# Optimization experiments

Measured on AMD Instinct MI355X. Metric: run time of the kernel, lower is better.

Reference implementation:

```python
import jax, jax.numpy as jnp
import numpy as np

WIN = 7       # window_size (square)
SHIFT = 3     # shift_size
HEADS = 4
WS = WIN * WIN  # 49 tokens per window


def _rel_index():
    # Swin relative position index, shape (WS*WS,), static ints
    coords = np.stack(np.meshgrid(np.arange(WIN), np.arange(WIN), indexing='ij'))
    cf = coords.reshape(2, -1)
    rel = (cf[:, :, None] - cf[:, None, :]).transpose(1, 2, 0)  # (WS, WS, 2)
    rel[:, :, 0] += WIN - 1
    rel[:, :, 1] += WIN - 1
    rel[:, :, 0] *= 2 * WIN - 1
    return rel.sum(-1).reshape(-1)

_REL_IDX = jnp.asarray(_rel_index())


def _attn_mask(H, W):
    # shift mask per window, shape (num_windows, WS, WS), static
    m = np.zeros((H, W), np.float32)
    cnt = 0
    for h in ((0, -WIN), (-WIN, -SHIFT), (-SHIFT, None)):
        for w in ((0, -WIN), (-WIN, -SHIFT), (-SHIFT, None)):
            m[h[0]:h[1], w[0]:w[1]] = cnt
            cnt += 1
    m = m.reshape(H // WIN, WIN, W // WIN, WIN).transpose(0, 2, 1, 3).reshape(-1, WS)
    diff = m[:, None, :] - m[:, :, None]
    return np.where(diff == 0, 0.0, -100.0).astype(np.float32)


def setup_inputs() -> dict:
    key = jax.random.key(0)
    ks = jax.random.split(key, 6)
    C = 128
    return {
        'x': jax.random.normal(ks[0], (64, 56, 56, C), jnp.float32),
        'qkv_kernel': jax.random.normal(ks[1], (C, 3 * C), jnp.float32) * (C ** -0.5),
        'qkv_bias': jax.random.normal(ks[2], (3 * C,), jnp.float32) * 0.02,
        'proj_kernel': jax.random.normal(ks[3], (C, C), jnp.float32) * (C ** -0.5),
        'proj_bias': jax.random.normal(ks[4], (C,), jnp.float32) * 0.02,
        'rel_pos_table': jax.random.normal(ks[5], ((2 * WIN - 1) ** 2, HEADS), jnp.float32) * 0.02,
    }


def reference(x, qkv_kernel, qkv_bias, proj_kernel, proj_bias, rel_pos_table):
    B, H, W, C = x.shape
    nH, nW = H // WIN, W // WIN
    head_dim = C // HEADS

    # cyclic shift + window partition -> (B*nH*nW, WS, C)
    xs = jnp.roll(x, (-SHIFT, -SHIFT), axis=(1, 2))
    xw = xs.reshape(B, nH, WIN, nW, WIN, C).transpose(0, 1, 3, 2, 4, 5).reshape(B * nH * nW, WS, C)

    qkv = xw @ qkv_kernel + qkv_bias
    qkv = qkv.reshape(-1, WS, 3, HEADS, head_dim).transpose(2, 0, 3, 1, 4)  # (3, n, h, WS, d)
    q, k, v = qkv[0], qkv[1], qkv[2]

    attn = jnp.einsum('nhsd,nhtd->nhst', q * head_dim ** -0.5, k)

    # relative position bias: (1, heads, WS, WS)
    bias = rel_pos_table[_REL_IDX].reshape(WS, WS, HEADS).transpose(2, 0, 1)[None]
    attn = attn + bias

    # shift mask (static)
    mask = jnp.asarray(_attn_mask(H, W))  # (nH*nW, WS, WS)
    attn = attn.reshape(B, nH * nW, HEADS, WS, WS) + mask[None, :, None]
    attn = jax.nn.softmax(attn.reshape(-1, HEADS, WS, WS), axis=-1)

    out = jnp.einsum('nhst,nhtd->nhsd', attn, v).transpose(0, 2, 1, 3).reshape(-1, WS, C)
    out = out @ proj_kernel + proj_bias

    # window merge + reverse shift
    out = out.reshape(B, nH, nW, WIN, WIN, C).transpose(0, 1, 3, 2, 4, 5).reshape(B, H, W, C)
    return jnp.roll(out, (SHIFT, SHIFT), axis=(1, 2))
```

## Files before the change

### kernel.cpp

```cpp
#include <hip/hip_runtime.h>
#include <hip/hip_bf16.h>

#define WIN 7
#define SHIFT_SZ 3
#define HEADS 4
#define WSQ 49
#define CH 128
#define HW 56

typedef short s16x8 __attribute__((ext_vector_type(8)));
typedef float f32x4 __attribute__((ext_vector_type(4)));


__global__ void prep_weights(const float* __restrict__ qkv_kernel,
                             const float* __restrict__ proj_kernel,
                             __hip_bfloat16* __restrict__ ws) {
  int idx = blockIdx.x * 256 + threadIdx.x;
  if (idx < 49152) {
    int n = idx >> 7, c = idx & 127;
    ws[idx] = __float2bfloat16(qkv_kernel[c * 384 + n]);
  }
  if (idx < 16384) {
    int n = idx >> 7, c = idx & 127;
    ws[49152 + idx] = __float2bfloat16(proj_kernel[c * 128 + n]);
  }
}

__global__ void prep_tbl(const float* __restrict__ rel_pos_table,
                         __hip_bfloat16* __restrict__ tbl) {
  int idx = blockIdx.x * 256 + threadIdx.x;
  int t = idx & 63;
  int s = (idx >> 6) & 63;
  int h = (idx >> 12) & 3;
  int win = idx >> 14;
  float v;
  if (t >= WSQ) v = -30000.f;
  else if (s >= WSQ) v = 0.f;
  else {
    int i1 = s / 7, j1 = s % 7, i2 = t / 7, j2 = t % 7;
    int ridx = (i1 - i2 + 6) * 13 + (j1 - j2 + 6);
    float bias = rel_pos_table[ridx * HEADS + h];
    int wy = win >> 3, wx = win & 7;
    int rh1 = (wy < 7) ? 0 : (i1 < 4 ? 1 : 2);
    int rh2 = (wy < 7) ? 0 : (i2 < 4 ? 1 : 2);
    int rw1 = (wx < 7) ? 0 : (j1 < 4 ? 1 : 2);
    int rw2 = (wx < 7) ? 0 : (j2 < 4 ? 1 : 2);
    float mask = (rh1 == rh2 && rw1 == rw2) ? 0.f : -100.f;
    v = bias + mask;
  }
  tbl[idx] = __float2bfloat16(v);
}


__launch_bounds__(512, 4)
__global__ void swin_attn(const float* __restrict__ x,
                          const float* __restrict__ qkv_bias,
                          const float* __restrict__ proj_bias,
                          const __hip_bfloat16* __restrict__ wqkvT,
                          const __hip_bfloat16* __restrict__ wprojT,
                          const __hip_bfloat16* __restrict__ tbl,
                          float* __restrict__ out) {
  __shared__ __align__(16) char smem[76800];
  __hip_bfloat16* a_lds  = (__hip_bfloat16*)smem;
  __hip_bfloat16* qk_lds = (__hip_bfloat16*)(smem + 17408);
  __hip_bfloat16* p_lds  = qk_lds;
  __hip_bfloat16* vt_lds = (__hip_bfloat16*)(smem + 58368);

  const int tid = threadIdx.x;
  const int lane = tid & 63;
  const int wv = tid >> 6;
  const int g = lane >> 4;
  const int c = lane & 15;

  const int widx = blockIdx.x;
  const int b  = widx >> 6;
  const int wy = (widx >> 3) & 7;
  const int wx = widx & 7;
  const int win64 = widx & 63;

  for (int it = tid; it < 1024; it += 512) {
    int s = it >> 4;
    int l16 = it & 15;
    union { s16x8 v; __hip_bfloat16 h[8]; } u;
    if (s < WSQ) {
      int i = s / 7, j = s - i * 7;
      int hh = wy * 7 + i + SHIFT_SZ; if (hh >= HW) hh -= HW;
      int ww = wx * 7 + j + SHIFT_SZ; if (ww >= HW) ww -= HW;
      const float4* src = (const float4*)(x + (((b * HW + hh) * HW + ww) * CH + l16 * 8));
      float4 f0 = src[0], f1 = src[1];
      u.h[0] = __float2bfloat16(f0.x); u.h[1] = __float2bfloat16(f0.y);
      u.h[2] = __float2bfloat16(f0.z); u.h[3] = __float2bfloat16(f0.w);
      u.h[4] = __float2bfloat16(f1.x); u.h[5] = __float2bfloat16(f1.y);
      u.h[6] = __float2bfloat16(f1.z); u.h[7] = __float2bfloat16(f1.w);
    } else {
      #pragma unroll
      for (int q = 0; q < 8; ++q) u.h[q] = __float2bfloat16(0.f);
    }
    *(s16x8*)(a_lds + s * 136 + l16 * 8) = u.v;
  }
  __syncthreads();

  {
    f32x4 acc[4][3];
    #pragma unroll
    for (int mt = 0; mt < 4; ++mt)
      #pragma unroll
      for (int ntl = 0; ntl < 3; ++ntl) acc[mt][ntl] = (f32x4){0.f, 0.f, 0.f, 0.f};

    #pragma unroll
    for (int kt = 0; kt < 4; ++kt) {
      s16x8 af[4];
      #pragma unroll
      for (int mt = 0; mt < 4; ++mt)
        af[mt] = *(const s16x8*)(a_lds + (16 * mt + c) * 136 + kt * 32 + g * 8);
      #pragma unroll
      for (int ntl = 0; ntl < 3; ++ntl) {
        int nt = 3 * wv + ntl;
        s16x8 bf = *(const s16x8*)(wqkvT + (16 * nt + c) * 128 + kt * 32 + g * 8);
        #pragma unroll
        for (int mt = 0; mt < 4; ++mt)
          acc[mt][ntl] = __builtin_amdgcn_mfma_f32_16x16x32_bf16(af[mt], bf, acc[mt][ntl], 0, 0, 0);
      }
    }
    #pragma unroll
    for (int ntl = 0; ntl < 3; ++ntl) {
      int nt = 3 * wv + ntl;
      int n = 16 * nt + c;
      float bias = qkv_bias[n];
      int sel = n >> 7;
      int rem = n & 127;
      int head = rem >> 5;
      int d = rem & 31;
      #pragma unroll
      for (int mt = 0; mt < 4; ++mt)
        #pragma unroll
        for (int r = 0; r < 4; ++r) {
          int s = 16 * mt + 4 * g + r;
          float v = acc[mt][ntl][r] + bias;
          if (sel == 0)
            qk_lds[(head * 64 + s) * 40 + d] = __float2bfloat16(v * 0.17677669529663687f);
          else if (sel == 1)
            qk_lds[10240 + (head * 64 + s) * 40 + d] = __float2bfloat16(v);
          else
            vt_lds[(head * 32 + d) * 72 + s] = __float2bfloat16(v);
        }
    }
  }
  __syncthreads();

  const int h = wv >> 1;
  const int mh = wv & 1;
  float den[2][4];
  f32x4 oacc[2][2];
  {
    s16x8 qf[2], kf[4];
    #pragma unroll
    for (int m = 0; m < 2; ++m)
      qf[m] = *(const s16x8*)(qk_lds + (h * 64 + 16 * (2 * mh + m) + c) * 40 + g * 8);
    #pragma unroll
    for (int nt = 0; nt < 4; ++nt)
      kf[nt] = *(const s16x8*)(qk_lds + 10240 + (h * 64 + 16 * nt + c) * 40 + g * 8);
    __syncthreads();

    f32x4 sacc[2][4];
    #pragma unroll
    for (int m = 0; m < 2; ++m)
      #pragma unroll
      for (int nt = 0; nt < 4; ++nt) {
        sacc[m][nt] = (f32x4){0.f, 0.f, 0.f, 0.f};
        sacc[m][nt] = __builtin_amdgcn_mfma_f32_16x16x32_bf16(qf[m], kf[nt], sacc[m][nt], 0, 0, 0);
      }

    const __hip_bfloat16* tb = tbl + (((win64 << 2) + h) << 12);
    #pragma unroll
    for (int m = 0; m < 2; ++m)
      #pragma unroll
      for (int nt = 0; nt < 4; ++nt)
        #pragma unroll
        for (int r = 0; r < 4; ++r) {
          int s = 16 * (2 * mh + m) + 4 * g + r;
          int t = 16 * nt + c;
          sacc[m][nt][r] += __bfloat162float(tb[(s << 6) + t]);
        }
    #pragma unroll
    for (int m = 0; m < 2; ++m)
      #pragma unroll
      for (int r = 0; r < 4; ++r) {
        float mx = fmaxf(fmaxf(sacc[m][0][r], sacc[m][1][r]), fmaxf(sacc[m][2][r], sacc[m][3][r]));
        #pragma unroll
        for (int off = 1; off < 16; off <<= 1) mx = fmaxf(mx, __shfl_xor(mx, off));
        float sum = 0.f;
        #pragma unroll
        for (int nt = 0; nt < 4; ++nt) {
          float e = __expf(sacc[m][nt][r] - mx);
          sacc[m][nt][r] = e;
          sum += e;
        }
        #pragma unroll
        for (int off = 1; off < 16; off <<= 1) sum += __shfl_xor(sum, off);
        den[m][r] = sum;
      }
    #pragma unroll
    for (int m = 0; m < 2; ++m)
      #pragma unroll
      for (int nt = 0; nt < 4; ++nt)
        #pragma unroll
        for (int r = 0; r < 4; ++r) {
          int s = 16 * (2 * mh + m) + 4 * g + r;
          int t = 16 * nt + c;
          p_lds[(h * 64 + s) * 72 + t] = __float2bfloat16(sacc[m][nt][r]);
        }
  }
  __syncthreads();

  #pragma unroll
  for (int m = 0; m < 2; ++m)
    #pragma unroll
    for (int ntd = 0; ntd < 2; ++ntd) oacc[m][ntd] = (f32x4){0.f, 0.f, 0.f, 0.f};
  #pragma unroll
  for (int kt = 0; kt < 2; ++kt) {
    s16x8 pf[2];
    #pragma unroll
    for (int m = 0; m < 2; ++m)
      pf[m] = *(const s16x8*)(p_lds + (h * 64 + 16 * (2 * mh + m) + c) * 72 + kt * 32 + g * 8);
    #pragma unroll
    for (int ntd = 0; ntd < 2; ++ntd) {
      s16x8 vf = *(const s16x8*)(vt_lds + (h * 32 + 16 * ntd + c) * 72 + kt * 32 + g * 8);
      #pragma unroll
      for (int m = 0; m < 2; ++m)
        oacc[m][ntd] = __builtin_amdgcn_mfma_f32_16x16x32_bf16(pf[m], vf, oacc[m][ntd], 0, 0, 0);
    }
  }
  #pragma unroll
  for (int m = 0; m < 2; ++m)
    #pragma unroll
    for (int ntd = 0; ntd < 2; ++ntd)
      #pragma unroll
      for (int r = 0; r < 4; ++r) {
        int s = 16 * (2 * mh + m) + 4 * g + r;
        int col = h * 32 + 16 * ntd + c;
        a_lds[s * 136 + col] = __float2bfloat16(oacc[m][ntd][r] / den[m][r]);
      }
  __syncthreads();

  {
    f32x4 pacc[4];
    #pragma unroll
    for (int mt = 0; mt < 4; ++mt) pacc[mt] = (f32x4){0.f, 0.f, 0.f, 0.f};
    #pragma unroll
    for (int kt = 0; kt < 4; ++kt) {
      s16x8 bfp = *(const s16x8*)(wprojT + (16 * wv + c) * 128 + kt * 32 + g * 8);
      #pragma unroll
      for (int mt = 0; mt < 4; ++mt) {
        s16x8 afo = *(const s16x8*)(a_lds + (16 * mt + c) * 136 + kt * 32 + g * 8);
        pacc[mt] = __builtin_amdgcn_mfma_f32_16x16x32_bf16(afo, bfp, pacc[mt], 0, 0, 0);
      }
    }
    float pb = proj_bias[16 * wv + c];
    #pragma unroll
    for (int mt = 0; mt < 4; ++mt)
      #pragma unroll
      for (int r = 0; r < 4; ++r) {
        int s = 16 * mt + 4 * g + r;
        if (s < WSQ) {
          int i = s / 7, j = s - i * 7;
          int hh = wy * 7 + i + SHIFT_SZ; if (hh >= HW) hh -= HW;
          int ww = wx * 7 + j + SHIFT_SZ; if (ww >= HW) ww -= HW;
          out[((b * HW + hh) * HW + ww) * CH + 16 * wv + c] = pacc[mt][r] + pb;
        }
      }
  }
}

extern "C" void kernel_launch(void* const* d_in, const int* in_sizes, int n_in,
                              void* d_out, int out_size, void* d_ws, size_t ws_size,
                              hipStream_t stream) {
  const float* x            = (const float*)d_in[0];
  const float* qkv_kernel   = (const float*)d_in[1];
  const float* qkv_bias     = (const float*)d_in[2];
  const float* proj_kernel  = (const float*)d_in[3];
  const float* proj_bias    = (const float*)d_in[4];
  const float* rel_pos_tbl  = (const float*)d_in[5];
  float* out = (float*)d_out;

  __hip_bfloat16* wsb    = (__hip_bfloat16*)d_ws;
  __hip_bfloat16* wqkvT  = wsb;
  __hip_bfloat16* wprojT = wsb + 49152;
  __hip_bfloat16* tbl    = wsb + 65536;

  prep_weights<<<dim3(192), dim3(256), 0, stream>>>(qkv_kernel, proj_kernel, wsb);
  prep_tbl<<<dim3(4096), dim3(256), 0, stream>>>(rel_pos_tbl, tbl);
  swin_attn<<<dim3(4096), dim3(512), 0, stream>>>(x, qkv_bias, proj_bias,
                                                  wqkvT, wprojT, tbl, out);
}
```

Before: 155.7 us.

## Transpose MFMA operand roles, shrink LDS, use exp2 softmax with folded scales

The QKV projection now computes Q/K transposed (weights as the A operand), so results are written to LDS as packed 4-element vectors. V^T uses an XOR-swizzled layout to avoid bank conflicts, and the projection output is stored as float4. Softmax runs per row inside a lane with only two cross-lane shuffles, uses exp2 with log2e folded into the q scale and the bias table, and normalises P before PV instead of dividing the output. The bias table is stored transposed. The LDS footprint is reduced from 76800 to 54272 bytes so the launch bound can rise to 6 blocks per CU. In exchange, bf16 rounding of the normalised probabilities shifts slightly.

```diff
diff --git a/kernel.cpp b/kernel.cpp
--- a/kernel.cpp
+++ b/kernel.cpp
@@ -3,12 +3,14 @@
 
 #define WIN 7
 #define SHIFT_SZ 3
-#define HEADS 4
 #define WSQ 49
 #define CH 128
 #define HW 56
+#define LOG2E 1.4426950408889634f
+#define QSCALE (0.17677669529663687f * LOG2E)
 
 typedef short s16x8 __attribute__((ext_vector_type(8)));
+typedef short s16x4 __attribute__((ext_vector_type(4)));
 typedef float f32x4 __attribute__((ext_vector_type(4)));
 
 
@@ -29,30 +31,37 @@
 __global__ void prep_tbl(const float* __restrict__ rel_pos_table,
                          __hip_bfloat16* __restrict__ tbl) {
   int idx = blockIdx.x * 256 + threadIdx.x;
-  int t = idx & 63;
-  int s = (idx >> 6) & 63;
+  int s = idx & 63;
+  int t = (idx >> 6) & 63;
   int h = (idx >> 12) & 3;
   int win = idx >> 14;
   float v;
-  if (t >= WSQ) v = -30000.f;
+  if (t >= WSQ) v = -43280.f;
   else if (s >= WSQ) v = 0.f;
   else {
     int i1 = s / 7, j1 = s % 7, i2 = t / 7, j2 = t % 7;
     int ridx = (i1 - i2 + 6) * 13 + (j1 - j2 + 6);
-    float bias = rel_pos_table[ridx * HEADS + h];
+    float bias = rel_pos_table[ridx * 4 + h];
     int wy = win >> 3, wx = win & 7;
     int rh1 = (wy < 7) ? 0 : (i1 < 4 ? 1 : 2);
     int rh2 = (wy < 7) ? 0 : (i2 < 4 ? 1 : 2);
     int rw1 = (wx < 7) ? 0 : (j1 < 4 ? 1 : 2);
     int rw2 = (wx < 7) ? 0 : (j2 < 4 ? 1 : 2);
     float mask = (rh1 == rh2 && rw1 == rw2) ? 0.f : -100.f;
-    v = bias + mask;
+    v = (bias + mask) * LOG2E;
   }
   tbl[idx] = __float2bfloat16(v);
 }
 
 
-__launch_bounds__(512, 4)
+static __device__ __forceinline__ s16x8 ld2x64(const __hip_bfloat16* p) {
+  s16x8 r;
+  *(s16x4*)&r = *(const s16x4*)p;
+  *(((s16x4*)&r) + 1) = *(const s16x4*)(p + 4);
+  return r;
+}
+
+__launch_bounds__(512, 6)
 __global__ void swin_attn(const float* __restrict__ x,
                           const float* __restrict__ qkv_bias,
                           const float* __restrict__ proj_bias,
@@ -60,11 +69,13 @@
                           const __hip_bfloat16* __restrict__ wprojT,
                           const __hip_bfloat16* __restrict__ tbl,
                           float* __restrict__ out) {
-  __shared__ __align__(16) char smem[76800];
+  __shared__ __align__(16) char smem[54272];
   __hip_bfloat16* a_lds  = (__hip_bfloat16*)smem;
-  __hip_bfloat16* qk_lds = (__hip_bfloat16*)(smem + 17408);
-  __hip_bfloat16* p_lds  = qk_lds;
-  __hip_bfloat16* vt_lds = (__hip_bfloat16*)(smem + 58368);
+  __hip_bfloat16* q_lds  = (__hip_bfloat16*)smem;
+  __hip_bfloat16* k_lds  = (__hip_bfloat16*)(smem + 18432);
+  __hip_bfloat16* vt_lds = (__hip_bfloat16*)(smem + 36864);
+  __hip_bfloat16* p_lds  = (__hip_bfloat16*)smem;
+  __hip_bfloat16* o_lds  = (__hip_bfloat16*)(smem + 36864);
 
   const int tid = threadIdx.x;
   const int lane = tid & 63;
@@ -100,135 +111,144 @@
   }
   __syncthreads();
 
+  f32x4 acc_qk[2][4];
+  f32x4 acc_v[4];
+  #pragma unroll
+  for (int ntl = 0; ntl < 2; ++ntl)
+    #pragma unroll
+    for (int mt = 0; mt < 4; ++mt) acc_qk[ntl][mt] = (f32x4){0.f, 0.f, 0.f, 0.f};
+  #pragma unroll
+  for (int mt = 0; mt < 4; ++mt) acc_v[mt] = (f32x4){0.f, 0.f, 0.f, 0.f};
+
+  #pragma unroll
+  for (int kt = 0; kt < 4; ++kt) {
+    s16x8 af[4];
+    #pragma unroll
+    for (int mt = 0; mt < 4; ++mt)
+      af[mt] = *(const s16x8*)(a_lds + (16 * mt + c) * 136 + kt * 32 + g * 8);
+    #pragma unroll
+    for (int ntl = 0; ntl < 2; ++ntl) {
+      s16x8 bf = *(const s16x8*)(wqkvT + (16 * (2 * wv + ntl) + c) * 128 + kt * 32 + g * 8);
+      #pragma unroll
+      for (int mt = 0; mt < 4; ++mt)
+        acc_qk[ntl][mt] = __builtin_amdgcn_mfma_f32_16x16x32_bf16(bf, af[mt], acc_qk[ntl][mt], 0, 0, 0);
+    }
+    s16x8 bv = *(const s16x8*)(wqkvT + (16 * (16 + wv) + c) * 128 + kt * 32 + g * 8);
+    #pragma unroll
+    for (int mt = 0; mt < 4; ++mt)
+      acc_v[mt] = __builtin_amdgcn_mfma_f32_16x16x32_bf16(af[mt], bv, acc_v[mt], 0, 0, 0);
+  }
+  __syncthreads();
+
   {
-    f32x4 acc[4][3];
-    #pragma unroll
-    for (int mt = 0; mt < 4; ++mt)
-      #pragma unroll
-      for (int ntl = 0; ntl < 3; ++ntl) acc[mt][ntl] = (f32x4){0.f, 0.f, 0.f, 0.f};
-
-    #pragma unroll
-    for (int kt = 0; kt < 4; ++kt) {
-      s16x8 af[4];
-      #pragma unroll
-      for (int mt = 0; mt < 4; ++mt)
-        af[mt] = *(const s16x8*)(a_lds + (16 * mt + c) * 136 + kt * 32 + g * 8);
-      #pragma unroll
-      for (int ntl = 0; ntl < 3; ++ntl) {
-        int nt = 3 * wv + ntl;
-        s16x8 bf = *(const s16x8*)(wqkvT + (16 * nt + c) * 128 + kt * 32 + g * 8);
-        #pragma unroll
-        for (int mt = 0; mt < 4; ++mt)
-          acc[mt][ntl] = __builtin_amdgcn_mfma_f32_16x16x32_bf16(af[mt], bf, acc[mt][ntl], 0, 0, 0);
+    const float scale = (wv < 4) ? QSCALE : 1.0f;
+    #pragma unroll
+    for (int ntl = 0; ntl < 2; ++ntl) {
+      int qt = 2 * wv + ntl;
+      int h = (qt >> 1) & 3;
+      int d0 = (qt & 1) * 16 + 4 * g;
+      float4 b4 = *(const float4*)(qkv_bias + qt * 16 + 4 * g);
+      __hip_bfloat16* dst = (qt < 8 ? q_lds : k_lds) + h * 64 * 36 + d0;
+      #pragma unroll
+      for (int mt = 0; mt < 4; ++mt) {
+        union { s16x4 v; __hip_bfloat16 h[4]; } u;
+        u.h[0] = __float2bfloat16((acc_qk[ntl][mt][0] + b4.x) * scale);
+        u.h[1] = __float2bfloat16((acc_qk[ntl][mt][1] + b4.y) * scale);
+        u.h[2] = __float2bfloat16((acc_qk[ntl][mt][2] + b4.z) * scale);
+        u.h[3] = __float2bfloat16((acc_qk[ntl][mt][3] + b4.w) * scale);
+        *(s16x4*)(dst + (16 * mt + c) * 36) = u.v;
       }
     }
-    #pragma unroll
-    for (int ntl = 0; ntl < 3; ++ntl) {
-      int nt = 3 * wv + ntl;
-      int n = 16 * nt + c;
-      float bias = qkv_bias[n];
-      int sel = n >> 7;
-      int rem = n & 127;
-      int head = rem >> 5;
-      int d = rem & 31;
-      #pragma unroll
-      for (int mt = 0; mt < 4; ++mt)
-        #pragma unroll
-        for (int r = 0; r < 4; ++r) {
-          int s = 16 * mt + 4 * g + r;
-          float v = acc[mt][ntl][r] + bias;
-          if (sel == 0)
-            qk_lds[(head * 64 + s) * 40 + d] = __float2bfloat16(v * 0.17677669529663687f);
-          else if (sel == 1)
-            qk_lds[10240 + (head * 64 + s) * 40 + d] = __float2bfloat16(v);
-          else
-            vt_lds[(head * 32 + d) * 72 + s] = __float2bfloat16(v);
-        }
-    }
-  }
-  __syncthreads();
-
-  const int h = wv >> 1;
+    int hv = wv >> 1;
+    int d = (wv & 1) * 16 + c;
+    float bv = qkv_bias[256 + wv * 16 + c];
+    __hip_bfloat16* vdst = vt_lds + (hv * 32 + d) * 64;
+    #pragma unroll
+    for (int mt = 0; mt < 4; ++mt) {
+      int s0 = 16 * mt + 4 * g;
+      union { s16x4 v; __hip_bfloat16 h[4]; } u;
+      #pragma unroll
+      for (int r = 0; r < 4; ++r) u.h[r] = __float2bfloat16(acc_v[mt][r] + bv);
+      *(s16x4*)(vdst + (((s0 >> 3) ^ (c & 7)) << 3) + (s0 & 7)) = u.v;
+    }
+  }
+  __syncthreads();
+
+  const int h3 = wv >> 1;
   const int mh = wv & 1;
-  float den[2][4];
+  s16x8 qf[2], kf[4], vf[2][2];
+  #pragma unroll
+  for (int m = 0; m < 2; ++m)
+    qf[m] = ld2x64(q_lds + (h3 * 64 + 16 * (2 * mh + m) + c) * 36 + g * 8);
+  #pragma unroll
+  for (int nt = 0; nt < 4; ++nt)
+    kf[nt] = ld2x64(k_lds + (h3 * 64 + 16 * nt + c) * 36 + g * 8);
+  #pragma unroll
+  for (int kt = 0; kt < 2; ++kt)
+    #pragma unroll
+    for (int ntd = 0; ntd < 2; ++ntd) {
+      int row = h3 * 32 + 16 * ntd + c;
+      int blk = (4 * kt + g) ^ (c & 7);
+      vf[kt][ntd] = *(const s16x8*)(vt_lds + row * 64 + blk * 8);
+    }
+  __syncthreads();
+
+  #pragma unroll
+  for (int m = 0; m < 2; ++m) {
+    f32x4 sc[4];
+    #pragma unroll
+    for (int nt = 0; nt < 4; ++nt) {
+      sc[nt] = (f32x4){0.f, 0.f, 0.f, 0.f};
+      sc[nt] = __builtin_amdgcn_mfma_f32_16x16x32_bf16(kf[nt], qf[m], sc[nt], 0, 0, 0);
+    }
+    const __hip_bfloat16* tb = tbl + (((win64 << 2) + h3) << 12) + 16 * (2 * mh + m) + c;
+    #pragma unroll
+    for (int nt = 0; nt < 4; ++nt)
+      #pragma unroll
+      for (int r = 0; r < 4; ++r)
+        sc[nt][r] += __bfloat162float(tb[(16 * nt + 4 * g + r) << 6]);
+    float mx = -1e30f;
+    #pragma unroll
+    for (int nt = 0; nt < 4; ++nt)
+      #pragma unroll
+      for (int r = 0; r < 4; ++r) mx = fmaxf(mx, sc[nt][r]);
+    mx = fmaxf(mx, __shfl_xor(mx, 16));
+    mx = fmaxf(mx, __shfl_xor(mx, 32));
+    float sum = 0.f;
+    #pragma unroll
+    for (int nt = 0; nt < 4; ++nt)
+      #pragma unroll
+      for (int r = 0; r < 4; ++r) {
+        float e = __builtin_amdgcn_exp2f(sc[nt][r] - mx);
+        sc[nt][r] = e;
+        sum += e;
+      }
+    sum += __shfl_xor(sum, 16);
+    sum += __shfl_xor(sum, 32);
+    float inv = __builtin_amdgcn_rcpf(sum);
+    __hip_bfloat16* prow = p_lds + (h3 * 64 + 16 * (2 * mh + m) + c) * 72;
+    #pragma unroll
+    for (int nt = 0; nt < 4; ++nt) {
+      union { s16x4 v; __hip_bfloat16 h[4]; } u;
+      #pragma unroll
+      for (int r = 0; r < 4; ++r) u.h[r] = __float2bfloat16(sc[nt][r] * inv);
+      *(s16x4*)(prow + 16 * nt + 4 * g) = u.v;
+    }
+  }
+
   f32x4 oacc[2][2];
-  {
-    s16x8 qf[2], kf[4];
-    #pragma unroll
-    for (int m = 0; m < 2; ++m)
-      qf[m] = *(const s16x8*)(qk_lds + (h * 64 + 16 * (2 * mh + m) + c) * 40 + g * 8);
-    #pragma unroll
-    for (int nt = 0; nt < 4; ++nt)
-      kf[nt] = *(const s16x8*)(qk_lds + 10240 + (h * 64 + 16 * nt + c) * 40 + g * 8);
-    __syncthreads();
-
-    f32x4 sacc[2][4];
-    #pragma unroll
-    for (int m = 0; m < 2; ++m)
-      #pragma unroll
-      for (int nt = 0; nt < 4; ++nt) {
-        sacc[m][nt] = (f32x4){0.f, 0.f, 0.f, 0.f};
-        sacc[m][nt] = __builtin_amdgcn_mfma_f32_16x16x32_bf16(qf[m], kf[nt], sacc[m][nt], 0, 0, 0);
-      }
-
-    const __hip_bfloat16* tb = tbl + (((win64 << 2) + h) << 12);
-    #pragma unroll
-    for (int m = 0; m < 2; ++m)
-      #pragma unroll
-      for (int nt = 0; nt < 4; ++nt)
-        #pragma unroll
-        for (int r = 0; r < 4; ++r) {
-          int s = 16 * (2 * mh + m) + 4 * g + r;
-          int t = 16 * nt + c;
-          sacc[m][nt][r] += __bfloat162float(tb[(s << 6) + t]);
-        }
-    #pragma unroll
-    for (int m = 0; m < 2; ++m)
-      #pragma unroll
-      for (int r = 0; r < 4; ++r) {
-        float mx = fmaxf(fmaxf(sacc[m][0][r], sacc[m][1][r]), fmaxf(sacc[m][2][r], sacc[m][3][r]));
-        #pragma unroll
-        for (int off = 1; off < 16; off <<= 1) mx = fmaxf(mx, __shfl_xor(mx, off));
-        float sum = 0.f;
-        #pragma unroll
-        for (int nt = 0; nt < 4; ++nt) {
-          float e = __expf(sacc[m][nt][r] - mx);
-          sacc[m][nt][r] = e;
-          sum += e;
-        }
-        #pragma unroll
-        for (int off = 1; off < 16; off <<= 1) sum += __shfl_xor(sum, off);
-        den[m][r] = sum;
-      }
-    #pragma unroll
-    for (int m = 0; m < 2; ++m)
-      #pragma unroll
-      for (int nt = 0; nt < 4; ++nt)
-        #pragma unroll
-        for (int r = 0; r < 4; ++r) {
-          int s = 16 * (2 * mh + m) + 4 * g + r;
-          int t = 16 * nt + c;
-          p_lds[(h * 64 + s) * 72 + t] = __float2bfloat16(sacc[m][nt][r]);
-        }
-  }
-  __syncthreads();
-
   #pragma unroll
   for (int m = 0; m < 2; ++m)
     #pragma unroll
     for (int ntd = 0; ntd < 2; ++ntd) oacc[m][ntd] = (f32x4){0.f, 0.f, 0.f, 0.f};
   #pragma unroll
   for (int kt = 0; kt < 2; ++kt) {
-    s16x8 pf[2];
-    #pragma unroll
-    for (int m = 0; m < 2; ++m)
-      pf[m] = *(const s16x8*)(p_lds + (h * 64 + 16 * (2 * mh + m) + c) * 72 + kt * 32 + g * 8);
-    #pragma unroll
-    for (int ntd = 0; ntd < 2; ++ntd) {
-      s16x8 vf = *(const s16x8*)(vt_lds + (h * 32 + 16 * ntd + c) * 72 + kt * 32 + g * 8);
-      #pragma unroll
-      for (int m = 0; m < 2; ++m)
-        oacc[m][ntd] = __builtin_amdgcn_mfma_f32_16x16x32_bf16(pf[m], vf, oacc[m][ntd], 0, 0, 0);
+    #pragma unroll
+    for (int m = 0; m < 2; ++m) {
+      s16x8 pf = *(const s16x8*)(p_lds + (h3 * 64 + 16 * (2 * mh + m) + c) * 72 + kt * 32 + g * 8);
+      #pragma unroll
+      for (int ntd = 0; ntd < 2; ++ntd)
+        oacc[m][ntd] = __builtin_amdgcn_mfma_f32_16x16x32_bf16(pf, vf[kt][ntd], oacc[m][ntd], 0, 0, 0);
     }
   }
   #pragma unroll
@@ -236,11 +256,9 @@
     #pragma unroll
     for (int ntd = 0; ntd < 2; ++ntd)
       #pragma unroll
-      for (int r = 0; r < 4; ++r) {
-        int s = 16 * (2 * mh + m) + 4 * g + r;
-        int col = h * 32 + 16 * ntd + c;
-        a_lds[s * 136 + col] = __float2bfloat16(oacc[m][ntd][r] / den[m][r]);
-      }
+      for (int r = 0; r < 4; ++r)
+        o_lds[(16 * (2 * mh + m) + 4 * g + r) * 136 + h3 * 32 + 16 * ntd + c] =
+            __float2bfloat16(oacc[m][ntd][r]);
   __syncthreads();
 
   {
@@ -252,23 +270,26 @@
       s16x8 bfp = *(const s16x8*)(wprojT + (16 * wv + c) * 128 + kt * 32 + g * 8);
       #pragma unroll
       for (int mt = 0; mt < 4; ++mt) {
-        s16x8 afo = *(const s16x8*)(a_lds + (16 * mt + c) * 136 + kt * 32 + g * 8);
-        pacc[mt] = __builtin_amdgcn_mfma_f32_16x16x32_bf16(afo, bfp, pacc[mt], 0, 0, 0);
+        s16x8 afo = *(const s16x8*)(o_lds + (16 * mt + c) * 136 + kt * 32 + g * 8);
+        pacc[mt] = __builtin_amdgcn_mfma_f32_16x16x32_bf16(bfp, afo, pacc[mt], 0, 0, 0);
       }
     }
-    float pb = proj_bias[16 * wv + c];
-    #pragma unroll
-    for (int mt = 0; mt < 4; ++mt)
-      #pragma unroll
-      for (int r = 0; r < 4; ++r) {
-        int s = 16 * mt + 4 * g + r;
-        if (s < WSQ) {
-          int i = s / 7, j = s - i * 7;
-          int hh = wy * 7 + i + SHIFT_SZ; if (hh >= HW) hh -= HW;
-          int ww = wx * 7 + j + SHIFT_SZ; if (ww >= HW) ww -= HW;
-          out[((b * HW + hh) * HW + ww) * CH + 16 * wv + c] = pacc[mt][r] + pb;
-        }
+    float4 pb4 = *(const float4*)(proj_bias + 16 * wv + 4 * g);
+    #pragma unroll
+    for (int mt = 0; mt < 4; ++mt) {
+      int s = 16 * mt + c;
+      if (s < WSQ) {
+        int i = s / 7, j = s - i * 7;
+        int hh = wy * 7 + i + SHIFT_SZ; if (hh >= HW) hh -= HW;
+        int ww = wx * 7 + j + SHIFT_SZ; if (ww >= HW) ww -= HW;
+        float4 v;
+        v.x = pacc[mt][0] + pb4.x;
+        v.y = pacc[mt][1] + pb4.y;
+        v.z = pacc[mt][2] + pb4.z;
+        v.w = pacc[mt][3] + pb4.w;
+        *(float4*)(out + ((b * HW + hh) * HW + ww) * CH + 16 * wv + 4 * g) = v;
       }
+    }
   }
 }
 
```

Result: slower. 220.7 us (+41.7%).
